# Optimization experiments

Measured on AMD Instinct MI355X. Metric: run time of the kernel, lower is better.

## Reference

```python
import jax, jax.numpy as jnp
import numpy as np

N_NODES = 100000
N_EDGES = 1600000
D_IN = 128
D_OUT = 128


def setup_inputs() -> dict:
    key = jax.random.key(0)
    k1, k2, k3 = jax.random.split(key, 3)
    x = jax.random.normal(k1, (N_NODES, D_IN), dtype=jnp.float32)
    edge_index = jax.random.randint(k2, (2, N_EDGES), 0, N_NODES, dtype=jnp.int64)
    # Glorot-style init for the GCN weight, zero bias (PyG defaults)
    W = jax.random.normal(k3, (D_IN, D_OUT), dtype=jnp.float32) * (1.0 / np.sqrt(D_IN))
    b = jnp.zeros((D_OUT,), dtype=jnp.float32)
    return {"x": x, "edge_index": edge_index, "W": W, "b": b}


def reference(x, edge_index, W, b):
    # GCNConv (PyG defaults: add_self_loops=True, normalize=True):
    #   out = D^{-1/2} (A + I) D^{-1/2} (X W) + b
    # Dropout is identity in eval mode.
    n = x.shape[0]
    loop = jnp.arange(n, dtype=edge_index.dtype)
    src = jnp.concatenate([edge_index[0], loop])  # [E + N]
    dst = jnp.concatenate([edge_index[1], loop])  # [E + N]

    h = x @ W  # [N, D_OUT] -- transform before aggregation (fewer FLOPs if D_OUT <= D_IN)

    # Degree of each node counting self-loops, computed over targets.
    ones = jnp.ones(dst.shape[0], dtype=h.dtype)
    deg = jax.ops.segment_sum(ones, dst, num_segments=n)  # [N]
    deg_inv_sqrt = jnp.where(deg > 0, jax.lax.rsqrt(deg), 0.0)

    # Symmetric normalization per edge: d_src^{-1/2} * d_dst^{-1/2}
    norm = deg_inv_sqrt[src] * deg_inv_sqrt[dst]  # [E + N]

    # Gather messages, scale, scatter-add to targets.
    msgs = h[src] * norm[:, None]  # [E + N, D_OUT]
    out = jax.ops.segment_sum(msgs, dst, num_segments=n)  # [N, D_OUT]
    return out + b
```

## Files before the change

### kernel.cpp

```cpp
#include <hip/hip_runtime.h>

#define DD 128
#define CAP 12288

typedef __attribute__((ext_vector_type(8))) short bf16x8;
typedef __attribute__((ext_vector_type(4))) float f32x4;

__device__ inline unsigned short f2b(float f) {
    unsigned int u = __float_as_uint(f);
    u += 0x7fffu + ((u >> 16) & 1u);
    return (unsigned short)(u >> 16);
}

__device__ inline void bacc16f(float4& a, float4& b, uint4 v, float s) {
    a.x += __uint_as_float(v.x << 16) * s;
    a.y += __uint_as_float(v.x & 0xffff0000u) * s;
    a.z += __uint_as_float(v.y << 16) * s;
    a.w += __uint_as_float(v.y & 0xffff0000u) * s;
    b.x += __uint_as_float(v.z << 16) * s;
    b.y += __uint_as_float(v.z & 0xffff0000u) * s;
    b.z += __uint_as_float(v.w << 16) * s;
    b.w += __uint_as_float(v.w & 0xffff0000u) * s;
}

__global__ __launch_bounds__(256) void k_pre(const float* __restrict__ W,
                                             unsigned short* __restrict__ Wt,
                                             int* __restrict__ cur, int nbuck) {
    int bid = blockIdx.x;
    if (bid < 64) {
        int idx = bid * 256 + threadIdx.x;
        int k = idx >> 7, c = idx & 127;
        Wt[c * DD + k] = f2b(W[k * DD + c]);
    } else {
        int b = (bid - 64) * 256 + threadIdx.x;
        if (b < nbuck) cur[b] = b * CAP;
    }
}

__global__ __launch_bounds__(256) void k_fA(const int* __restrict__ src,
                                            const int* __restrict__ dst, int E,
                                            int chunk, int nbuck,
                                            int* __restrict__ cur,
                                            int* __restrict__ binned,
                                            const float* __restrict__ x,
                                            const unsigned short* __restrict__ Wt,
                                            unsigned short* __restrict__ hs,
                                            int n, int ngA) {
    const int t = threadIdx.x;
    if ((int)blockIdx.x >= ngA) {
        __shared__ int hist[256];
        __shared__ int base[256];
        __shared__ int curs[256];
        const int e0 = (blockIdx.x - ngA) * chunk;
        const int e1 = min(e0 + chunk, E);

        if (t < 256) { hist[t] = 0; curs[t] = 0; }
        __syncthreads();
        for (int e = e0 + t * 4; e < e1; e += 1024) {
            int4 d4 = *(const int4*)(dst + e);
            atomicAdd(&hist[d4.x >> 9], 1);
            atomicAdd(&hist[d4.y >> 9], 1);
            atomicAdd(&hist[d4.z >> 9], 1);
            atomicAdd(&hist[d4.w >> 9], 1);
        }
        __syncthreads();
        if (t < nbuck && hist[t] > 0)
            base[t] = atomicAdd(&cur[t], hist[t]);
        __syncthreads();
        for (int e = e0 + t * 4; e < e1; e += 1024) {
            int4 d4 = *(const int4*)(dst + e);
            int4 s4 = *(const int4*)(src + e);
            {
                int b = d4.x >> 9, p = atomicAdd(&curs[b], 1), idx = base[b] + p;
                if (idx < (b + 1) * CAP) binned[idx] = (s4.x << 9) | (d4.x & 511);
            }
            {
                int b = d4.y >> 9, p = atomicAdd(&curs[b], 1), idx = base[b] + p;
                if (idx < (b + 1) * CAP) binned[idx] = (s4.y << 9) | (d4.y & 511);
            }
            {
                int b = d4.z >> 9, p = atomicAdd(&curs[b], 1), idx = base[b] + p;
                if (idx < (b + 1) * CAP) binned[idx] = (s4.z << 9) | (d4.z & 511);
            }
            {
                int b = d4.w >> 9, p = atomicAdd(&curs[b], 1), idx = base[b] + p;
                if (idx < (b + 1) * CAP) binned[idx] = (s4.w << 9) | (d4.w & 511);
            }
        }
        return;
    }

    const int wave = t >> 6, lane = t & 63;
    const int rowbase = blockIdx.x * 256 + wave * 64;
    const int l15 = lane & 15, l4 = lane >> 4;

    bf16x8 a[4][4];
    #pragma unroll
    for (int rb = 0; rb < 4; ++rb) {
        int r = rowbase + rb * 16 + l15;
        int rc = min(r, n - 1);
        const float* xr = x + (size_t)rc * DD;
        #pragma unroll
        for (int kc = 0; kc < 4; ++kc) {
            int k0 = kc * 32 + l4 * 8;
            float4 f0 = *(const float4*)(xr + k0);
            float4 f1 = *(const float4*)(xr + k0 + 4);
            bf16x8 fr;
            fr[0] = (short)f2b(f0.x); fr[1] = (short)f2b(f0.y);
            fr[2] = (short)f2b(f0.z); fr[3] = (short)f2b(f0.w);
            fr[4] = (short)f2b(f1.x); fr[5] = (short)f2b(f1.y);
            fr[6] = (short)f2b(f1.z); fr[7] = (short)f2b(f1.w);
            a[rb][kc] = fr;
        }
    }

    #pragma unroll
    for (int cb = 0; cb < 8; ++cb) {
        int c0 = cb * 16;
        f32x4 acc[4] = {};
        #pragma unroll
        for (int kc = 0; kc < 4; ++kc) {
            bf16x8 bfrag = *(const bf16x8*)(Wt + (size_t)(c0 + l15) * DD + kc * 32 + l4 * 8);
            #pragma unroll
            for (int rb = 0; rb < 4; ++rb)
                acc[rb] = __builtin_amdgcn_mfma_f32_16x16x32_bf16(a[rb][kc], bfrag, acc[rb], 0, 0, 0);
        }
        #pragma unroll
        for (int rb = 0; rb < 4; ++rb) {
            int r0 = rowbase + rb * 16 + l4 * 4;
            #pragma unroll
            for (int vv = 0; vv < 4; ++vv) {
                int r = r0 + vv;
                if (r < n)
                    hs[(size_t)r * DD + c0 + l15] = f2b(acc[rb][vv]);
            }
        }
    }
}

__global__ __launch_bounds__(512) void k_fB(int* __restrict__ binned,
                                            const int* __restrict__ cur,
                                            int* __restrict__ off,
                                            int* __restrict__ cnt,
                                            float* __restrict__ dinv,
                                            const float* __restrict__ x,
                                            const unsigned short* __restrict__ Wt,
                                            unsigned short* __restrict__ hs,
                                            int n, int nbuck, int growoff) {
    __shared__ int hist[512];
    __shared__ int curs[512];
    __shared__ int wsum[8];
    __shared__ int sorted[CAP];
    const int t = threadIdx.x;

    if (blockIdx.x < (unsigned)nbuck) {
        const int b = blockIdx.x;
        const int base = b * CAP;
        const int cb = cur[b] - base;
        const int cb4 = cb & ~3;
        const int lane = t & 63, w = t >> 6;

        hist[t] = 0;
        __syncthreads();
        for (int i = t * 4; i < cb4; i += 2048) {
            int4 v4 = *(const int4*)(binned + base + i);
            atomicAdd(&hist[v4.x & 511], 1);
            atomicAdd(&hist[v4.y & 511], 1);
            atomicAdd(&hist[v4.z & 511], 1);
            atomicAdd(&hist[v4.w & 511], 1);
        }
        if (t < cb - cb4)
            atomicAdd(&hist[binned[base + cb4 + t] & 511], 1);
        __syncthreads();
        int v = hist[t];
        int incl = v;
        #pragma unroll
        for (int m = 1; m < 64; m <<= 1) {
            int up = __shfl_up(incl, m);
            if (lane >= m) incl += up;
        }
        if (lane == 63) wsum[w] = incl;
        __syncthreads();
        int wpre = 0;
        #pragma unroll
        for (int j = 0; j < 8; ++j)
            wpre += (j < w) ? wsum[j] : 0;
        int excl = wpre + incl - v;
        curs[t] = excl;
        int d = b * 512 + t;
        if (d < n) {
            off[d]  = base + excl;
            cnt[d]  = v;
            dinv[d] = rsqrtf((float)v + 1.0f);
        }
        __syncthreads();
        for (int i = t * 4; i < cb4; i += 2048) {
            int4 p4 = *(const int4*)(binned + base + i);
            int p;
            p = atomicAdd(&curs[p4.x & 511], 1); sorted[p] = p4.x >> 9;
            p = atomicAdd(&curs[p4.y & 511], 1); sorted[p] = p4.y >> 9;
            p = atomicAdd(&curs[p4.z & 511], 1); sorted[p] = p4.z >> 9;
            p = atomicAdd(&curs[p4.w & 511], 1); sorted[p] = p4.w >> 9;
        }
        if (t < cb - cb4) {
            int pk = binned[base + cb4 + t];
            int p = atomicAdd(&curs[pk & 511], 1); sorted[p] = pk >> 9;
        }
        __syncthreads();
        for (int i = t * 4; i < cb4; i += 2048)
            *(int4*)(binned + base + i) = *(const int4*)(sorted + i);
        if (t < cb - cb4)
            binned[base + cb4 + t] = sorted[cb4 + t];
        return;
    }

    const int gb = blockIdx.x - nbuck;
    const int wave = t >> 6, lane = t & 63;
    const int rowbase = growoff + gb * 256 + wave * 32;
    const int l15 = lane & 15, l4 = lane >> 4;

    bf16x8 a[2][4];
    #pragma unroll
    for (int rb = 0; rb < 2; ++rb) {
        int r = rowbase + rb * 16 + l15;
        int rc = min(r, n - 1);
        const float* xr = x + (size_t)rc * DD;
        #pragma unroll
        for (int kc = 0; kc < 4; ++kc) {
            int k0 = kc * 32 + l4 * 8;
            float4 f0 = *(const float4*)(xr + k0);
            float4 f1 = *(const float4*)(xr + k0 + 4);
            bf16x8 fr;
            fr[0] = (short)f2b(f0.x); fr[1] = (short)f2b(f0.y);
            fr[2] = (short)f2b(f0.z); fr[3] = (short)f2b(f0.w);
            fr[4] = (short)f2b(f1.x); fr[5] = (short)f2b(f1.y);
            fr[6] = (short)f2b(f1.z); fr[7] = (short)f2b(f1.w);
            a[rb][kc] = fr;
        }
    }

    #pragma unroll
    for (int cb8 = 0; cb8 < 8; ++cb8) {
        int c0 = cb8 * 16;
        f32x4 acc[2] = {};
        #pragma unroll
        for (int kc = 0; kc < 4; ++kc) {
            bf16x8 bfrag = *(const bf16x8*)(Wt + (size_t)(c0 + l15) * DD + kc * 32 + l4 * 8);
            #pragma unroll
            for (int rb = 0; rb < 2; ++rb)
                acc[rb] = __builtin_amdgcn_mfma_f32_16x16x32_bf16(a[rb][kc], bfrag, acc[rb], 0, 0, 0);
        }
        #pragma unroll
        for (int rb = 0; rb < 2; ++rb) {
            int r0 = rowbase + rb * 16 + l4 * 4;
            #pragma unroll
            for (int vv = 0; vv < 4; ++vv) {
                int r = r0 + vv;
                if (r < n)
                    hs[(size_t)r * DD + c0 + l15] = f2b(acc[rb][vv]);
            }
        }
    }
}

__global__ __launch_bounds__(256, 8) void k_agg(const uint4* __restrict__ hsr,
                                                const int* __restrict__ ssrc,
                                                const int* __restrict__ off,
                                                const int* __restrict__ cnt,
                                                const float* __restrict__ dinv,
                                                const float* __restrict__ bias,
                                                float* __restrict__ out, int n) {
    const int t = threadIdx.x;
    const int wave = t >> 6, lane = t & 63;
    const int q  = lane >> 4;
    const int ql = lane & 15;
    const int d = blockIdx.x * 4 + wave;
    if (d >= n) return;

    const int s0 = off[d];
    const int c  = cnt[d];
    const float di = dinv[d];

    float4 accA = {0.f, 0.f, 0.f, 0.f};
    float4 accB = {0.f, 0.f, 0.f, 0.f};

    uint4 vself = hsr[(size_t)d * 16 + ql];

    int idx[6];
    #pragma unroll
    for (int r = 0; r < 6; ++r) {
        int e = r * 4 + q;
        idx[r] = ssrc[s0 + ((e < c) ? e : 0)];
    }
    #pragma unroll
    for (int r = 0; r < 6; ++r) {
        int e = r * 4 + q;
        idx[r] = (e < c) ? idx[r] : d;
    }

    uint4 val[6];
    float sc[6];
    #pragma unroll
    for (int r = 0; r < 6; ++r) {
        val[r] = hsr[(size_t)idx[r] * 16 + ql];
        sc[r]  = dinv[idx[r]];
    }

    if (q == 0) bacc16f(accA, accB, vself, di);
    #pragma unroll
    for (int r = 0; r < 6; ++r) {
        int e = r * 4 + q;
        if (e < c) bacc16f(accA, accB, val[r], sc[r]);
    }

    for (int i = 24 + q; i < c; i += 4) {
        int s = ssrc[s0 + i];
        uint4 v = hsr[(size_t)s * 16 + ql];
        bacc16f(accA, accB, v, dinv[s]);
    }

    #pragma unroll
    for (int m = 16; m <= 32; m <<= 1) {
        accA.x += __shfl_xor(accA.x, m);
        accA.y += __shfl_xor(accA.y, m);
        accA.z += __shfl_xor(accA.z, m);
        accA.w += __shfl_xor(accA.w, m);
        accB.x += __shfl_xor(accB.x, m);
        accB.y += __shfl_xor(accB.y, m);
        accB.z += __shfl_xor(accB.z, m);
        accB.w += __shfl_xor(accB.w, m);
    }

    if (q == 0) {
        float4 b0 = ((const float4*)bias)[ql * 2];
        float4 b1 = ((const float4*)bias)[ql * 2 + 1];
        float4 o0, o1;
        o0.x = accA.x * di + b0.x;
        o0.y = accA.y * di + b0.y;
        o0.z = accA.z * di + b0.z;
        o0.w = accA.w * di + b0.w;
        o1.x = accB.x * di + b1.x;
        o1.y = accB.y * di + b1.y;
        o1.z = accB.z * di + b1.z;
        o1.w = accB.w * di + b1.w;
        float4* orow = (float4*)(out + (size_t)d * DD);
        orow[ql * 2]     = o0;
        orow[ql * 2 + 1] = o1;
    }
}

extern "C" void kernel_launch(void* const* d_in, const int* in_sizes, int n_in,
                              void* d_out, int out_size, void* d_ws, size_t ws_size,
                              hipStream_t stream) {
    const float* x  = (const float*)d_in[0];
    const int*   ei = (const int*)d_in[1];
    const float* W  = (const float*)d_in[2];
    const float* b  = (const float*)d_in[3];
    float* out = (float*)d_out;

    const int n = in_sizes[0] / DD;
    const int E = in_sizes[1] / 2;
    const int* src = ei;
    const int* dst = ei + E;

    const int nbuck = (n + 511) >> 9;

    unsigned short* hs = (unsigned short*)d_ws;
    unsigned short* Wt = hs + (size_t)n * DD;
    int*   binned = (int*)(Wt + DD * DD);
    int*   off    = binned + (size_t)nbuck * CAP;
    int*   cnt    = off + n;
    float* dinv   = (float*)(cnt + n);
    int*   cur    = (int*)(dinv + n);

    const int nblkA = 256;
    const int chunk = (((E + nblkA - 1) / nblkA) + 3) & ~3;

    const int ngA = 195;
    const int growoff = ngA * 256;
    const int ngB = (n - growoff + 255) / 256;

    k_pre<<<64 + (nbuck + 255) / 256, 256, 0, stream>>>(W, Wt, cur, nbuck);
    k_fA <<<ngA + nblkA, 256, 0, stream>>>(src, dst, E, chunk, nbuck, cur, binned,
                                           x, Wt, hs, n, ngA);
    k_fB <<<nbuck + ngB, 512, 0, stream>>>(binned, cur, off, cnt, dinv,
                                           x, Wt, hs, n, nbuck, growoff);
    k_agg<<<(n + 3) / 4, 256, 0, stream>>>((const uint4*)hs, binned, off, cnt,
                                           dinv, b, out, n);
}
```

Before: 112.1 us.

## Fold weight transpose into GEMM blocks via LDS and drop pre-kernel

Removes the separate k_pre kernel. Each GEMM block now converts and transposes W to bf16 into a padded LDS tile shared by union with the binning scratch, and bucket cursors are zeroed with a memset and treated as relative offsets. The k_fB GEMM blocks are also enlarged to 512 rows with 4 row-blocks per wave. This saves one kernel launch and the global Wt round trip, but every GEMM block now redoes the 128x128 W conversion and uses more LDS, which may lower occupancy.

```diff
diff --git a/kernel.cpp b/kernel.cpp
--- a/kernel.cpp
+++ b/kernel.cpp
@@ -2,6 +2,7 @@
 
 #define DD 128
 #define CAP 12288
+#define WP 136
 
 typedef __attribute__((ext_vector_type(8))) short bf16x8;
 typedef __attribute__((ext_vector_type(4))) float f32x4;
@@ -23,19 +24,10 @@
     b.w += __uint_as_float(v.w & 0xffff0000u) * s;
 }
 
-__global__ __launch_bounds__(256) void k_pre(const float* __restrict__ W,
-                                             unsigned short* __restrict__ Wt,
-                                             int* __restrict__ cur, int nbuck) {
-    int bid = blockIdx.x;
-    if (bid < 64) {
-        int idx = bid * 256 + threadIdx.x;
-        int k = idx >> 7, c = idx & 127;
-        Wt[c * DD + k] = f2b(W[k * DD + c]);
-    } else {
-        int b = (bid - 64) * 256 + threadIdx.x;
-        if (b < nbuck) cur[b] = b * CAP;
-    }
-}
+union UA {
+    struct { int hist[256]; int base[256]; int curs[256]; } a;
+    unsigned short wlds[DD * WP];
+};
 
 __global__ __launch_bounds__(256) void k_fA(const int* __restrict__ src,
                                             const int* __restrict__ dst, int E,
@@ -43,52 +35,56 @@
                                             int* __restrict__ cur,
                                             int* __restrict__ binned,
                                             const float* __restrict__ x,
-                                            const unsigned short* __restrict__ Wt,
+                                            const float* __restrict__ W,
                                             unsigned short* __restrict__ hs,
                                             int n, int ngA) {
+    __shared__ UA u;
     const int t = threadIdx.x;
     if ((int)blockIdx.x >= ngA) {
-        __shared__ int hist[256];
-        __shared__ int base[256];
-        __shared__ int curs[256];
         const int e0 = (blockIdx.x - ngA) * chunk;
         const int e1 = min(e0 + chunk, E);
 
-        if (t < 256) { hist[t] = 0; curs[t] = 0; }
+        u.a.hist[t] = 0; u.a.curs[t] = 0;
         __syncthreads();
         for (int e = e0 + t * 4; e < e1; e += 1024) {
             int4 d4 = *(const int4*)(dst + e);
-            atomicAdd(&hist[d4.x >> 9], 1);
-            atomicAdd(&hist[d4.y >> 9], 1);
-            atomicAdd(&hist[d4.z >> 9], 1);
-            atomicAdd(&hist[d4.w >> 9], 1);
-        }
-        __syncthreads();
-        if (t < nbuck && hist[t] > 0)
-            base[t] = atomicAdd(&cur[t], hist[t]);
+            atomicAdd(&u.a.hist[d4.x >> 9], 1);
+            atomicAdd(&u.a.hist[d4.y >> 9], 1);
+            atomicAdd(&u.a.hist[d4.z >> 9], 1);
+            atomicAdd(&u.a.hist[d4.w >> 9], 1);
+        }
+        __syncthreads();
+        if (t < nbuck && u.a.hist[t] > 0)
+            u.a.base[t] = t * CAP + atomicAdd(&cur[t], u.a.hist[t]);
         __syncthreads();
         for (int e = e0 + t * 4; e < e1; e += 1024) {
             int4 d4 = *(const int4*)(dst + e);
             int4 s4 = *(const int4*)(src + e);
             {
-                int b = d4.x >> 9, p = atomicAdd(&curs[b], 1), idx = base[b] + p;
+                int b = d4.x >> 9, p = atomicAdd(&u.a.curs[b], 1), idx = u.a.base[b] + p;
                 if (idx < (b + 1) * CAP) binned[idx] = (s4.x << 9) | (d4.x & 511);
             }
             {
-                int b = d4.y >> 9, p = atomicAdd(&curs[b], 1), idx = base[b] + p;
+                int b = d4.y >> 9, p = atomicAdd(&u.a.curs[b], 1), idx = u.a.base[b] + p;
                 if (idx < (b + 1) * CAP) binned[idx] = (s4.y << 9) | (d4.y & 511);
             }
             {
-                int b = d4.z >> 9, p = atomicAdd(&curs[b], 1), idx = base[b] + p;
+                int b = d4.z >> 9, p = atomicAdd(&u.a.curs[b], 1), idx = u.a.base[b] + p;
                 if (idx < (b + 1) * CAP) binned[idx] = (s4.z << 9) | (d4.z & 511);
             }
             {
-                int b = d4.w >> 9, p = atomicAdd(&curs[b], 1), idx = base[b] + p;
+                int b = d4.w >> 9, p = atomicAdd(&u.a.curs[b], 1), idx = u.a.base[b] + p;
                 if (idx < (b + 1) * CAP) binned[idx] = (s4.w << 9) | (d4.w & 511);
             }
         }
         return;
     }
+
+    for (int i = t; i < DD * DD; i += 256) {
+        int k = i >> 7, c = i & 127;
+        u.wlds[c * WP + k] = f2b(W[i]);
+    }
+    __syncthreads();
 
     const int wave = t >> 6, lane = t & 63;
     const int rowbase = blockIdx.x * 256 + wave * 64;
@@ -120,7 +116,7 @@
         f32x4 acc[4] = {};
         #pragma unroll
         for (int kc = 0; kc < 4; ++kc) {
-            bf16x8 bfrag = *(const bf16x8*)(Wt + (size_t)(c0 + l15) * DD + kc * 32 + l4 * 8);
+            bf16x8 bfrag = *(const bf16x8*)(&u.wlds[(c0 + l15) * WP + kc * 32 + l4 * 8]);
             #pragma unroll
             for (int rb = 0; rb < 4; ++rb)
                 acc[rb] = __builtin_amdgcn_mfma_f32_16x16x32_bf16(a[rb][kc], bfrag, acc[rb], 0, 0, 0);
@@ -138,25 +134,30 @@
     }
 }
 
+union UB {
+    int sorted[CAP];
+    unsigned short wlds[DD * WP];
+};
+
 __global__ __launch_bounds__(512) void k_fB(int* __restrict__ binned,
                                             const int* __restrict__ cur,
                                             int* __restrict__ off,
                                             int* __restrict__ cnt,
                                             float* __restrict__ dinv,
                                             const float* __restrict__ x,
-                                            const unsigned short* __restrict__ Wt,
+                                            const float* __restrict__ W,
                                             unsigned short* __restrict__ hs,
                                             int n, int nbuck, int growoff) {
     __shared__ int hist[512];
     __shared__ int curs[512];
     __shared__ int wsum[8];
-    __shared__ int sorted[CAP];
+    __shared__ UB ub;
     const int t = threadIdx.x;
 
     if (blockIdx.x < (unsigned)nbuck) {
         const int b = blockIdx.x;
         const int base = b * CAP;
-        const int cb = cur[b] - base;
+        const int cb = min(cur[b], CAP);
         const int cb4 = cb & ~3;
         const int lane = t & 63, w = t >> 6;
 
@@ -197,31 +198,37 @@
         for (int i = t * 4; i < cb4; i += 2048) {
             int4 p4 = *(const int4*)(binned + base + i);
             int p;
-            p = atomicAdd(&curs[p4.x & 511], 1); sorted[p] = p4.x >> 9;
-            p = atomicAdd(&curs[p4.y & 511], 1); sorted[p] = p4.y >> 9;
-            p = atomicAdd(&curs[p4.z & 511], 1); sorted[p] = p4.z >> 9;
-            p = atomicAdd(&curs[p4.w & 511], 1); sorted[p] = p4.w >> 9;
+            p = atomicAdd(&curs[p4.x & 511], 1); ub.sorted[p] = p4.x >> 9;
+            p = atomicAdd(&curs[p4.y & 511], 1); ub.sorted[p] = p4.y >> 9;
+            p = atomicAdd(&curs[p4.z & 511], 1); ub.sorted[p] = p4.z >> 9;
+            p = atomicAdd(&curs[p4.w & 511], 1); ub.sorted[p] = p4.w >> 9;
         }
         if (t < cb - cb4) {
             int pk = binned[base + cb4 + t];
-            int p = atomicAdd(&curs[pk & 511], 1); sorted[p] = pk >> 9;
+            int p = atomicAdd(&curs[pk & 511], 1); ub.sorted[p] = pk >> 9;
         }
         __syncthreads();
         for (int i = t * 4; i < cb4; i += 2048)
-            *(int4*)(binned + base + i) = *(const int4*)(sorted + i);
+            *(int4*)(binned + base + i) = *(const int4*)(ub.sorted + i);
         if (t < cb - cb4)
-            binned[base + cb4 + t] = sorted[cb4 + t];
+            binned[base + cb4 + t] = ub.sorted[cb4 + t];
         return;
     }
+
+    for (int i = t; i < DD * DD; i += 512) {
+        int k = i >> 7, c = i & 127;
+        ub.wlds[c * WP + k] = f2b(W[i]);
+    }
+    __syncthreads();
 
     const int gb = blockIdx.x - nbuck;
     const int wave = t >> 6, lane = t & 63;
-    const int rowbase = growoff + gb * 256 + wave * 32;
+    const int rowbase = growoff + gb * 512 + wave * 64;
     const int l15 = lane & 15, l4 = lane >> 4;
 
-    bf16x8 a[2][4];
-    #pragma unroll
-    for (int rb = 0; rb < 2; ++rb) {
+    bf16x8 a[4][4];
+    #pragma unroll
+    for (int rb = 0; rb < 4; ++rb) {
         int r = rowbase + rb * 16 + l15;
         int rc = min(r, n - 1);
         const float* xr = x + (size_t)rc * DD;
@@ -242,16 +249,16 @@
     #pragma unroll
     for (int cb8 = 0; cb8 < 8; ++cb8) {
         int c0 = cb8 * 16;
-        f32x4 acc[2] = {};
+        f32x4 acc[4] = {};
         #pragma unroll
         for (int kc = 0; kc < 4; ++kc) {
-            bf16x8 bfrag = *(const bf16x8*)(Wt + (size_t)(c0 + l15) * DD + kc * 32 + l4 * 8);
+            bf16x8 bfrag = *(const bf16x8*)(&ub.wlds[(c0 + l15) * WP + kc * 32 + l4 * 8]);
             #pragma unroll
-            for (int rb = 0; rb < 2; ++rb)
+            for (int rb = 0; rb < 4; ++rb)
                 acc[rb] = __builtin_amdgcn_mfma_f32_16x16x32_bf16(a[rb][kc], bfrag, acc[rb], 0, 0, 0);
         }
         #pragma unroll
-        for (int rb = 0; rb < 2; ++rb) {
+        for (int rb = 0; rb < 4; ++rb) {
             int r0 = rowbase + rb * 16 + l4 * 4;
             #pragma unroll
             for (int vv = 0; vv < 4; ++vv) {
@@ -366,8 +373,7 @@
     const int nbuck = (n + 511) >> 9;
 
     unsigned short* hs = (unsigned short*)d_ws;
-    unsigned short* Wt = hs + (size_t)n * DD;
-    int*   binned = (int*)(Wt + DD * DD);
+    int*   binned = (int*)(hs + (size_t)n * DD);
     int*   off    = binned + (size_t)nbuck * CAP;
     int*   cnt    = off + n;
     float* dinv   = (float*)(cnt + n);
@@ -378,13 +384,13 @@
 
     const int ngA = 195;
     const int growoff = ngA * 256;
-    const int ngB = (n - growoff + 255) / 256;
-
-    k_pre<<<64 + (nbuck + 255) / 256, 256, 0, stream>>>(W, Wt, cur, nbuck);
+    const int ngB = (n - growoff + 511) / 512;
+
+    hipMemsetAsync(cur, 0, (size_t)nbuck * sizeof(int), stream);
     k_fA <<<ngA + nblkA, 256, 0, stream>>>(src, dst, E, chunk, nbuck, cur, binned,
-                                           x, Wt, hs, n, ngA);
+                                           x, W, hs, n, ngA);
     k_fB <<<nbuck + ngB, 512, 0, stream>>>(binned, cur, off, cnt, dinv,
-                                           x, Wt, hs, n, nbuck, growoff);
+                                           x, W, hs, n, nbuck, growoff);
     k_agg<<<(n + 3) / 4, 256, 0, stream>>>((const uint4*)hs, binned, off, cnt,
                                            dinv, b, out, n);
 }
```

Result: slower. 116.6 us (+4.1%).
